# Kernel optimization log

Measured on AMD Instinct MI355X. Metric: run time of the kernel, lower is better.

The kernel has to match this reference:

```python
import jax, jax.numpy as jnp
import numpy as np

N_USER, N_ITEM, D = 50000, 30000, 64
N = N_USER + N_ITEM
NNZ_UI, NNZ_R, NNZ_II = 1000000, 800000, 300000
IMG_F, TXT_F = 512, 384
EPS = 1e-5


def spmm(rows, cols, vals, x, n_out):
    # sparse [n_out, n_in] @ dense [n_in, d] via gather + segment-sum
    return jax.ops.segment_sum(vals[:, None] * x[cols], rows, num_segments=n_out)


def leaky_relu(x):
    return jnp.where(x >= 0, x, 0.01 * x)


def setup_inputs() -> dict:
    key = jax.random.key(0)
    ks = jax.random.split(key, 32)
    f = lambda i, shape, s=0.05: (jax.random.normal(ks[i], shape, dtype=jnp.float32) * s)
    inp = {
        'user_emb': f(0, (N_USER, D)),
        'item_emb': f(1, (N_ITEM, D)),
        'image_embedding': f(2, (N_ITEM, IMG_F), 1.0),
        'text_embedding': f(3, (N_ITEM, TXT_F), 1.0),
        'W_img': f(4, (IMG_F, D)), 'b_img': jnp.zeros((D,), jnp.float32),
        'bn_g_img': jnp.ones((D,), jnp.float32), 'bn_b_img': jnp.zeros((D,), jnp.float32),
        'W_txt': f(5, (TXT_F, D)), 'b_txt': jnp.zeros((D,), jnp.float32),
        'bn_g_txt': jnp.ones((D,), jnp.float32), 'bn_b_txt': jnp.zeros((D,), jnp.float32),
        'W_gate_img': f(6, (D, D)), 'b_gate_img': jnp.zeros((D,), jnp.float32),
        'W_gate_txt': f(7, (D, D)), 'b_gate_txt': jnp.zeros((D,), jnp.float32),
        'W_common1': f(8, (D, D)), 'b_common1': jnp.zeros((D,), jnp.float32),
        'w_common2': f(9, (D,)),
        'ui_vals': jax.random.uniform(ks[10], (NNZ_UI,), dtype=jnp.float32),
        'R_vals': jax.random.uniform(ks[11], (NNZ_R,), dtype=jnp.float32),
        'ii_img_vals': jax.random.uniform(ks[12], (NNZ_II,), dtype=jnp.float32),
        'ii_txt_vals': jax.random.uniform(ks[13], (NNZ_II,), dtype=jnp.float32),
        'ui_rows': jax.random.randint(ks[14], (NNZ_UI,), 0, N, dtype=jnp.int32),
        'ui_cols': jax.random.randint(ks[15], (NNZ_UI,), 0, N, dtype=jnp.int32),
        'R_rows': jax.random.randint(ks[16], (NNZ_R,), 0, N_USER, dtype=jnp.int32),
        'R_cols': jax.random.randint(ks[17], (NNZ_R,), 0, N_ITEM, dtype=jnp.int32),
        'ii_img_rows': jax.random.randint(ks[18], (NNZ_II,), 0, N_ITEM, dtype=jnp.int32),
        'ii_img_cols': jax.random.randint(ks[19], (NNZ_II,), 0, N_ITEM, dtype=jnp.int32),
        'ii_txt_rows': jax.random.randint(ks[20], (NNZ_II,), 0, N_ITEM, dtype=jnp.int32),
        'ii_txt_cols': jax.random.randint(ks[21], (NNZ_II,), 0, N_ITEM, dtype=jnp.int32),
    }
    return inp


def reference(user_emb, item_emb, image_embedding, text_embedding,
              W_img, b_img, bn_g_img, bn_b_img,
              W_txt, b_txt, bn_g_txt, bn_b_txt,
              W_gate_img, b_gate_img, W_gate_txt, b_gate_txt,
              W_common1, b_common1, w_common2,
              ui_vals, R_vals, ii_img_vals, ii_txt_vals,
              ui_rows, ui_cols, R_rows, R_cols,
              ii_img_rows, ii_img_cols, ii_txt_rows, ii_txt_cols):
    # ---- user_item_GCN: adj = original + diffusion (fused edge list) ----
    cat = jnp.concatenate([item_emb, user_emb], axis=0)  # [N, D], item first per source
    embs = [cat]
    for _ in range(2):
        cat = spmm(ui_rows, ui_cols, ui_vals, cat, N)
        embs.append(cat)
    content_embedding = jnp.stack(embs, axis=1).mean(axis=1)  # [N, D]

    # ---- modal projections (BN inference, dropout=eval identity) ----
    def project(x, W, b, g, beta):
        h = x @ W + b
        h = h * (g / jnp.sqrt(1.0 + EPS)) + beta  # BatchNorm1d, running stats (0, 1)
        return leaky_relu(h)

    img_feat = project(image_embedding, W_img, b_img, bn_g_img, bn_b_img)  # [I, D]
    txt_feat = project(text_embedding, W_txt, b_txt, bn_g_txt, bn_b_txt)

    # ---- item_item_GCN ----
    def modal_branch(feat, Wg, bg, rows, cols, vals):
        it = item_emb * jax.nn.sigmoid(feat @ Wg + bg)  # gated item embedding
        for _ in range(2):
            it = spmm(rows, cols, vals, it, N_ITEM)
        us = spmm(R_rows, R_cols, R_vals, it, N_USER)  # R @ item -> user
        return jnp.concatenate([us, it], axis=0)  # [N, D], user first per source

    image_ui = modal_branch(img_feat, W_gate_img, b_gate_img, ii_img_rows, ii_img_cols, ii_img_vals)
    text_ui = modal_branch(txt_feat, W_gate_txt, b_gate_txt, ii_txt_rows, ii_txt_cols, ii_txt_vals)

    # ---- gate_attention_fusion (non-tiktok: 2 modalities) ----
    def att_score(e):
        return leaky_relu(e @ W_common1 + b_common1) @ w_common2  # [N]

    att = jnp.stack([att_score(image_ui), att_score(text_ui)], axis=-1)  # [N, 2]
    w = jax.nn.softmax(att, axis=-1)
    common = w[:, 0:1] * image_ui + w[:, 1:2] * text_ui
    special_img = image_ui - common
    special_txt = text_ui - common

    return jnp.stack([content_embedding, special_img, special_txt, common], axis=0)  # [4, N, D]
```

## Files before the change

### kernel.cpp

```cpp
#include <hip/hip_runtime.h>

#define N_USER 50000
#define N_ITEM 30000
#define DIM    64
#define NTOT   80000
#define NNZ_UI 1000000
#define NNZ_R  800000
#define NNZ_II 300000
#define IMG_F  512
#define TXT_F  384

#define NROWS_ALL 190000
#define NNZ_ALL   2400000
#define BASE_R    NTOT
#define BASE_II   (NTOT + N_USER)
#define BASE_IT   (NTOT + N_USER + N_ITEM)

#define RB_BITS   9
#define RB_ROWS   512
#define NBUCK     ((NROWS_ALL + RB_ROWS - 1) / RB_ROWS)
#define NBLK_A2   400
#define EDG_A2    6000

__device__ __forceinline__ int edge_row(int i,
        const int* __restrict__ r0, const int* __restrict__ r1,
        const int* __restrict__ r2, const int* __restrict__ r3){
    if (i < NNZ_UI)                       return r0[i];
    if (i < NNZ_UI + NNZ_R)               return BASE_R  + r1[i - NNZ_UI];
    if (i < NNZ_UI + NNZ_R + NNZ_II)      return BASE_II + r2[i - NNZ_UI - NNZ_R];
    return BASE_IT + r3[i - NNZ_UI - NNZ_R - NNZ_II];
}

__device__ __forceinline__ void edge_all(int i,
        const int* __restrict__ r0, const int* __restrict__ c0, const float* __restrict__ v0,
        const int* __restrict__ r1, const int* __restrict__ c1, const float* __restrict__ v1,
        const int* __restrict__ r2, const int* __restrict__ c2, const float* __restrict__ v2,
        const int* __restrict__ r3, const int* __restrict__ c3, const float* __restrict__ v3,
        int& gr, int& col, float& val){
    if (i < NNZ_UI){
        gr = r0[i]; col = c0[i]; val = v0[i];
    } else if (i < NNZ_UI + NNZ_R){
        int j = i - NNZ_UI;               gr = BASE_R  + r1[j]; col = c1[j]; val = v1[j];
    } else if (i < NNZ_UI + NNZ_R + NNZ_II){
        int j = i - NNZ_UI - NNZ_R;       gr = BASE_II + r2[j]; col = c2[j]; val = v2[j];
    } else {
        int j = i - NNZ_UI - NNZ_R - NNZ_II; gr = BASE_IT + r3[j]; col = c3[j]; val = v3[j];
    }
}

__global__ __launch_bounds__(256) void k_bhist(const int* __restrict__ r0,
        const int* __restrict__ r1, const int* __restrict__ r2,
        const int* __restrict__ r3, int* __restrict__ bcnt){
    __shared__ int h[NBUCK];
    for (int i = threadIdx.x; i < NBUCK; i += 256) h[i] = 0;
    __syncthreads();
    const int stride = gridDim.x * 256;
    for (int i = blockIdx.x * 256 + threadIdx.x; i < NNZ_ALL; i += stride){
        int gr = edge_row(i, r0, r1, r2, r3);
        atomicAdd(&h[gr >> RB_BITS], 1);
    }
    __syncthreads();
    for (int i = threadIdx.x; i < NBUCK; i += 256){
        int c = h[i];
        if (c) atomicAdd(&bcnt[i], c);
    }
}

__global__ __launch_bounds__(512) void k_bscan(const int* __restrict__ bcnt,
        int* __restrict__ bbase, int* __restrict__ off){
    __shared__ int sh[512];
    const int t = threadIdx.x;
    int v = (t < NBUCK) ? bcnt[t] : 0;
    sh[t] = v;
    __syncthreads();
    for (int d = 1; d < 512; d <<= 1){
        int u = (t >= d) ? sh[t - d] : 0;
        __syncthreads();
        sh[t] += u;
        __syncthreads();
    }
    if (t < NBUCK) bbase[t] = sh[t] - v;
    if (t == NBUCK - 1){
        bbase[NBUCK] = sh[t];
        off[NROWS_ALL] = sh[t];
    }
}

__global__ __launch_bounds__(256) void k_bin(
        const int* __restrict__ r0, const int* __restrict__ c0, const float* __restrict__ v0,
        const int* __restrict__ r1, const int* __restrict__ c1, const float* __restrict__ v1,
        const int* __restrict__ r2, const int* __restrict__ c2, const float* __restrict__ v2,
        const int* __restrict__ r3, const int* __restrict__ c3, const float* __restrict__ v3,
        const int* __restrict__ bbase, int* __restrict__ bcur,
        int2* __restrict__ binned){
    __shared__ int lofs[NBUCK];
    __shared__ int lcur[NBUCK];
    const int t = threadIdx.x;
    for (int i = t; i < NBUCK; i += 256){ lofs[i] = 0; lcur[i] = 0; }
    __syncthreads();
    const int s0 = blockIdx.x * EDG_A2, s1 = s0 + EDG_A2;
    for (int i = s0 + t; i < s1; i += 256){
        int gr = edge_row(i, r0, r1, r2, r3);
        atomicAdd(&lofs[gr >> RB_BITS], 1);
    }
    __syncthreads();
    for (int i = t; i < NBUCK; i += 256){
        int c = lofs[i];
        lofs[i] = c ? (bbase[i] + atomicAdd(&bcur[i], c)) : 0;
    }
    __syncthreads();
    for (int i = s0 + t; i < s1; i += 256){
        int gr, col; float val;
        edge_all(i, r0, c0, v0, r1, c1, v1, r2, c2, v2, r3, c3, v3, gr, col, val);
        int b = gr >> RB_BITS;
        int slot = atomicAdd(&lcur[b], 1);
        binned[lofs[b] + slot] = make_int2((col << RB_BITS) | (gr & (RB_ROWS - 1)),
                                           __float_as_int(val));
    }
}

__global__ __launch_bounds__(256) void k_scatter(const int* __restrict__ bbase,
        const int2* __restrict__ binned, int* __restrict__ off,
        int2* __restrict__ csr){
    __shared__ int h[RB_ROWS];
    const int t = threadIdx.x;
    const int b = blockIdx.x;
    const int base = bbase[b];
    const int nb = bbase[b + 1] - base;
    h[t] = 0; h[t + 256] = 0;
    __syncthreads();
    for (int i = t; i < nb; i += 256)
        atomicAdd(&h[binned[base + i].x & (RB_ROWS - 1)], 1);
    __syncthreads();
    if (t < 64){
        int v[8], s = 0;
#pragma unroll
        for (int k = 0; k < 8; ++k){ v[k] = h[t * 8 + k]; s += v[k]; }
        int incl = s;
#pragma unroll
        for (int d = 1; d < 64; d <<= 1){
            int u = __shfl_up(incl, d, 64);
            if (t >= d) incl += u;
        }
        int run = incl - s;
#pragma unroll
        for (int k = 0; k < 8; ++k){ int tmp = v[k]; h[t * 8 + k] = run; run += tmp; }
    }
    __syncthreads();
    const int row0 = b << RB_BITS;
    for (int i = t; i < RB_ROWS; i += 256){
        int r = row0 + i;
        if (r < NROWS_ALL) off[r] = base + h[i];
    }
    __syncthreads();
    for (int i = t; i < nb; i += 256){
        int2 rec = binned[base + i];
        int lr = rec.x & (RB_ROWS - 1);
        int slot = atomicAdd(&h[lr], 1);
        csr[base + slot] = make_int2(rec.x >> RB_BITS, rec.y);
    }
}

__global__ void k_cat0(const float* __restrict__ item, const float* __restrict__ user,
                       float* __restrict__ o1){
    int i = blockIdx.x * 256 + threadIdx.x;
    const int ITEMS = N_ITEM * DIM;
    o1[i] = (i < ITEMS) ? item[i] : user[i - ITEMS];
}

__global__ void k_pull(const int* __restrict__ off, const int2* __restrict__ csr,
                       const float* __restrict__ x, float* __restrict__ y, int nrows){
    int t = blockIdx.x * 256 + threadIdx.x;
    int r = t >> 4;
    if (r >= nrows) return;
    int l = (t & 15) << 2;
    int s = off[r], e = off[r + 1];
    float4 a0 = {0.f, 0.f, 0.f, 0.f};
    float4 a1 = {0.f, 0.f, 0.f, 0.f};
    int j = s;
    for (; j + 2 <= e; j += 2){
        int2 e0 = csr[j];
        int2 e1 = csr[j + 1];
        float v0 = __int_as_float(e0.y);
        float v1 = __int_as_float(e1.y);
        const float4 x0 = *reinterpret_cast<const float4*>(x + ((long)e0.x << 6) + l);
        const float4 x1 = *reinterpret_cast<const float4*>(x + ((long)e1.x << 6) + l);
        a0.x = fmaf(v0, x0.x, a0.x);
        a0.y = fmaf(v0, x0.y, a0.y);
        a0.z = fmaf(v0, x0.z, a0.z);
        a0.w = fmaf(v0, x0.w, a0.w);
        a1.x = fmaf(v1, x1.x, a1.x);
        a1.y = fmaf(v1, x1.y, a1.y);
        a1.z = fmaf(v1, x1.z, a1.z);
        a1.w = fmaf(v1, x1.w, a1.w);
    }
    if (j < e){
        int2 e0 = csr[j];
        float v0 = __int_as_float(e0.y);
        const float4 x0 = *reinterpret_cast<const float4*>(x + ((long)e0.x << 6) + l);
        a0.x = fmaf(v0, x0.x, a0.x);
        a0.y = fmaf(v0, x0.y, a0.y);
        a0.z = fmaf(v0, x0.z, a0.z);
        a0.w = fmaf(v0, x0.w, a0.w);
    }
    a0.x += a1.x; a0.y += a1.y; a0.z += a1.z; a0.w += a1.w;
    *reinterpret_cast<float4*>(y + ((long)r << 6) + l) = a0;
}

__global__ void k_content(const float* __restrict__ a, const float* __restrict__ b,
                          const float* __restrict__ c, float* __restrict__ o0){
    int i = blockIdx.x * 256 + threadIdx.x;
    o0[i] = (a[i] + b[i] + c[i]) * (1.0f / 3.0f);
}

template<int K>
__global__ __launch_bounds__(256) void k_projgate(
        const float* __restrict__ X,
        const float* __restrict__ W,  const float* __restrict__ b,
        const float* __restrict__ g,  const float* __restrict__ beta,
        const float* __restrict__ Wg, const float* __restrict__ bg,
        const float* __restrict__ item, float* __restrict__ outP){
    __shared__ float xs[48][68];
    __shared__ float ws[64][64];
    const int t  = threadIdx.x;
    const int tr = t >> 4;
    const int tc = t & 15;
    const int row0 = blockIdx.x * 48;

    float acc[3][4];
#pragma unroll
    for (int i = 0; i < 3; ++i)
#pragma unroll
        for (int j = 0; j < 4; ++j) acc[i][j] = 0.f;

    for (int ks = 0; ks < K; ks += 64){
        __syncthreads();
#pragma unroll
        for (int i = 0; i < 3; ++i){
            int r = tr + 16 * i;
            *reinterpret_cast<float4*>(&xs[r][tc * 4]) =
                *reinterpret_cast<const float4*>(X + (long)(row0 + r) * K + ks + tc * 4);
        }
        {
            const float4* wsrc = reinterpret_cast<const float4*>(W + (long)ks * 64);
            float4* wdst = reinterpret_cast<float4*>(&ws[0][0]);
#pragma unroll
            for (int i = 0; i < 4; ++i) wdst[t + 256 * i] = wsrc[t + 256 * i];
        }
        __syncthreads();
#pragma unroll 8
        for (int kk = 0; kk < 64; kk += 2){
            float2 a[3];
#pragma unroll
            for (int i = 0; i < 3; ++i)
                a[i] = *reinterpret_cast<const float2*>(&xs[tr + 16 * i][kk]);
            float4 b0 = *reinterpret_cast<const float4*>(&ws[kk][tc * 4]);
            float4 b1 = *reinterpret_cast<const float4*>(&ws[kk + 1][tc * 4]);
#pragma unroll
            for (int i = 0; i < 3; ++i){
                acc[i][0] = fmaf(a[i].x, b0.x, acc[i][0]);
                acc[i][1] = fmaf(a[i].x, b0.y, acc[i][1]);
                acc[i][2] = fmaf(a[i].x, b0.z, acc[i][2]);
                acc[i][3] = fmaf(a[i].x, b0.w, acc[i][3]);
                acc[i][0] = fmaf(a[i].y, b1.x, acc[i][0]);
                acc[i][1] = fmaf(a[i].y, b1.y, acc[i][1]);
                acc[i][2] = fmaf(a[i].y, b1.z, acc[i][2]);
                acc[i][3] = fmaf(a[i].y, b1.w, acc[i][3]);
            }
        }
    }

    const float4 b4  = reinterpret_cast<const float4*>(b)[tc];
    const float4 g4  = reinterpret_cast<const float4*>(g)[tc];
    const float4 be4 = reinterpret_cast<const float4*>(beta)[tc];
    __syncthreads();
#pragma unroll
    for (int i = 0; i < 3; ++i){
        int r = tr + 16 * i;
        float4 h;
        h.x = (acc[i][0] + b4.x) * (g4.x * 0.99999500003749943f) + be4.x;
        h.y = (acc[i][1] + b4.y) * (g4.y * 0.99999500003749943f) + be4.y;
        h.z = (acc[i][2] + b4.z) * (g4.z * 0.99999500003749943f) + be4.z;
        h.w = (acc[i][3] + b4.w) * (g4.w * 0.99999500003749943f) + be4.w;
        h.x = (h.x >= 0.f) ? h.x : 0.01f * h.x;
        h.y = (h.y >= 0.f) ? h.y : 0.01f * h.y;
        h.z = (h.z >= 0.f) ? h.z : 0.01f * h.z;
        h.w = (h.w >= 0.f) ? h.w : 0.01f * h.w;
        *reinterpret_cast<float4*>(&xs[r][tc * 4]) = h;
    }
    {
        const float4* wsrc = reinterpret_cast<const float4*>(Wg);
        float4* wdst = reinterpret_cast<float4*>(&ws[0][0]);
#pragma unroll
        for (int i = 0; i < 4; ++i) wdst[t + 256 * i] = wsrc[t + 256 * i];
    }
    __syncthreads();

    float ac2[3][4];
#pragma unroll
    for (int i = 0; i < 3; ++i)
#pragma unroll
        for (int j = 0; j < 4; ++j) ac2[i][j] = 0.f;
#pragma unroll 8
    for (int kk = 0; kk < 64; kk += 2){
        float2 a[3];
#pragma unroll
        for (int i = 0; i < 3; ++i)
            a[i] = *reinterpret_cast<const float2*>(&xs[tr + 16 * i][kk]);
        float4 b0 = *reinterpret_cast<const float4*>(&ws[kk][tc * 4]);
        float4 b1 = *reinterpret_cast<const float4*>(&ws[kk + 1][tc * 4]);
#pragma unroll
        for (int i = 0; i < 3; ++i){
            ac2[i][0] = fmaf(a[i].x, b0.x, ac2[i][0]);
            ac2[i][1] = fmaf(a[i].x, b0.y, ac2[i][1]);
            ac2[i][2] = fmaf(a[i].x, b0.z, ac2[i][2]);
            ac2[i][3] = fmaf(a[i].x, b0.w, ac2[i][3]);
            ac2[i][0] = fmaf(a[i].y, b1.x, ac2[i][0]);
            ac2[i][1] = fmaf(a[i].y, b1.y, ac2[i][1]);
            ac2[i][2] = fmaf(a[i].y, b1.z, ac2[i][2]);
            ac2[i][3] = fmaf(a[i].y, b1.w, ac2[i][3]);
        }
    }

    const float4 bg4 = reinterpret_cast<const float4*>(bg)[tc];
#pragma unroll
    for (int i = 0; i < 3; ++i){
        int r = tr + 16 * i;
        const float4 iv = *reinterpret_cast<const float4*>(
                item + (long)(row0 + r) * 64 + tc * 4);
        float4 o;
        o.x = iv.x / (1.f + __expf(-(ac2[i][0] + bg4.x)));
        o.y = iv.y / (1.f + __expf(-(ac2[i][1] + bg4.y)));
        o.z = iv.z / (1.f + __expf(-(ac2[i][2] + bg4.z)));
        o.w = iv.w / (1.f + __expf(-(ac2[i][3] + bg4.w)));
        *reinterpret_cast<float4*>(outP + (long)(row0 + r) * 64 + tc * 4) = o;
    }
}

__global__ void k_copy(const float* __restrict__ s, float* __restrict__ d){
    int i = blockIdx.x * 256 + threadIdx.x;
    d[i] = s[i];
}

__global__ __launch_bounds__(256) void k_fuse(const float* __restrict__ img,
        const float* __restrict__ txt, const float* __restrict__ W1,
        const float* __restrict__ b1, const float* __restrict__ w2,
        float* __restrict__ out){
    __shared__ float si[4][64], st[4][64];
    const int t = threadIdx.x;
    const int w = t >> 6, c = t & 63;
    const long row = (long)blockIdx.x * 4 + w;
    float ie = img[row * 64 + c];
    float te = txt[row * 64 + c];
    si[w][c] = ie;  st[w][c] = te;
    __syncthreads();
    float ai = 0.f, at = 0.f;
#pragma unroll
    for (int k = 0; k < 64; ++k){
        float wv = W1[k * 64 + c];
        ai = fmaf(si[w][k], wv, ai);
        at = fmaf(st[w][k], wv, at);
    }
    float bb = b1[c];
    float hi = ai + bb; hi = (hi >= 0.f) ? hi : 0.01f * hi;
    float ht = at + bb; ht = (ht >= 0.f) ? ht : 0.01f * ht;
    float wc = w2[c];
    float pi = hi * wc, pt = ht * wc;
#pragma unroll
    for (int m = 1; m < 64; m <<= 1){
        pi += __shfl_xor(pi, m, 64);
        pt += __shfl_xor(pt, m, 64);
    }
    float mx = fmaxf(pi, pt);
    float ei = __expf(pi - mx), et = __expf(pt - mx);
    float inv = 1.f / (ei + et);
    float wi = ei * inv, wt = et * inv;
    float common = wi * ie + wt * te;
    const long NTD = (long)NTOT * DIM;
    long o = row * 64 + c;
    out[NTD + o]     = ie - common;
    out[2 * NTD + o] = te - common;
    out[3 * NTD + o] = common;
}

extern "C" void kernel_launch(void* const* d_in, const int* in_sizes, int n_in,
                              void* d_out, int out_size, void* d_ws, size_t ws_size,
                              hipStream_t stream){
    const float* user_emb  = (const float*)d_in[0];
    const float* item_emb  = (const float*)d_in[1];
    const float* image_emb = (const float*)d_in[2];
    const float* text_emb  = (const float*)d_in[3];
    const float* W_img = (const float*)d_in[4];
    const float* b_img = (const float*)d_in[5];
    const float* g_img = (const float*)d_in[6];
    const float* be_img= (const float*)d_in[7];
    const float* W_txt = (const float*)d_in[8];
    const float* b_txt = (const float*)d_in[9];
    const float* g_txt = (const float*)d_in[10];
    const float* be_txt= (const float*)d_in[11];
    const float* W_gi  = (const float*)d_in[12];
    const float* b_gi  = (const float*)d_in[13];
    const float* W_gt  = (const float*)d_in[14];
    const float* b_gt  = (const float*)d_in[15];
    const float* W_c1  = (const float*)d_in[16];
    const float* b_c1  = (const float*)d_in[17];
    const float* w_c2  = (const float*)d_in[18];
    const float* ui_vals = (const float*)d_in[19];
    const float* R_vals  = (const float*)d_in[20];
    const float* ii_iv   = (const float*)d_in[21];
    const float* ii_tv   = (const float*)d_in[22];
    const int* ui_rows = (const int*)d_in[23];
    const int* ui_cols = (const int*)d_in[24];
    const int* R_rows  = (const int*)d_in[25];
    const int* R_cols  = (const int*)d_in[26];
    const int* ii_ir   = (const int*)d_in[27];
    const int* ii_ic   = (const int*)d_in[28];
    const int* ii_tr   = (const int*)d_in[29];
    const int* ii_tc   = (const int*)d_in[30];

    const long ND = (long)NTOT * DIM;
    const long ID = (long)N_ITEM * DIM;
    const long UD = (long)N_USER * DIM;

    float* out = (float*)d_out;
    float* o0 = out;
    float* o1 = out + ND;
    float* o2 = out + 2 * ND;
    float* o3 = out + 3 * ND;

    float* P = o3;
    float* Q = o3 + ID;

    int2* binned = (int2*)o0;

    int2* csr   = (int2*)d_ws;
    int*  off   = (int*)(csr + NNZ_ALL);
    int*  bcnt  = off + NROWS_ALL + 4;
    int*  bcur  = bcnt + NBUCK;
    int*  bbase = bcur + NBUCK;

    hipMemsetAsync(bcnt, 0, 2 * NBUCK * sizeof(int), stream);
    k_bhist<<<512, 256, 0, stream>>>(ui_rows, R_rows, ii_ir, ii_tr, bcnt);
    k_bscan<<<1, 512, 0, stream>>>(bcnt, bbase, off);
    k_bin<<<NBLK_A2, 256, 0, stream>>>(
        ui_rows, ui_cols, ui_vals,  R_rows, R_cols, R_vals,
        ii_ir, ii_ic, ii_iv,        ii_tr, ii_tc, ii_tv,
        bbase, bcur, binned);
    k_scatter<<<NBUCK, 256, 0, stream>>>(bbase, binned, off, csr);

    const int* offUI = off;
    const int* offR  = off + BASE_R;
    const int* offI2 = off + BASE_II;
    const int* offT2 = off + BASE_IT;

    k_cat0<<<ND / 256, 256, 0, stream>>>(item_emb, user_emb, o1);
    k_pull<<<NTOT / 16, 256, 0, stream>>>(offUI, csr, o1, o2, NTOT);
    k_pull<<<NTOT / 16, 256, 0, stream>>>(offUI, csr, o2, o3, NTOT);
    k_content<<<ND / 256, 256, 0, stream>>>(o1, o2, o3, o0);

    k_projgate<IMG_F><<<N_ITEM / 48, 256, 0, stream>>>(
        image_emb, W_img, b_img, g_img, be_img, W_gi, b_gi, item_emb, P);
    k_pull<<<N_ITEM / 16, 256, 0, stream>>>(offI2, csr, P, Q, N_ITEM);
    k_pull<<<N_ITEM / 16, 256, 0, stream>>>(offI2, csr, Q, P, N_ITEM);
    k_pull<<<N_USER / 16, 256, 0, stream>>>(offR, csr, P, o1, N_USER);
    k_copy<<<ID / 256, 256, 0, stream>>>(P, o1 + UD);

    k_projgate<TXT_F><<<N_ITEM / 48, 256, 0, stream>>>(
        text_emb, W_txt, b_txt, g_txt, be_txt, W_gt, b_gt, item_emb, P);
    k_pull<<<N_ITEM / 16, 256, 0, stream>>>(offT2, csr, P, Q, N_ITEM);
    k_pull<<<N_ITEM / 16, 256, 0, stream>>>(offT2, csr, Q, P, N_ITEM);
    k_pull<<<N_USER / 16, 256, 0, stream>>>(offR, csr, P, o2, N_USER);
    k_copy<<<ID / 256, 256, 0, stream>>>(P, o2 + UD);

    k_fuse<<<NTOT / 4, 256, 0, stream>>>(o1, o2, W_c1, b_c1, w_c2, out);
}
```

Measured before the change: 636.7 us.

## Fuse content mean into second pull, drop copies, register-tile attention fusion

The second UI propagation pass now computes the three-layer mean in the same kernel, which removes the separate content kernel and the write and reread of o3. The second item-item pull now writes straight into the concat buffers, so the two copy kernels go away. The attention fusion kernel is rewritten to handle 64 rows per block, with W1 staged in shared memory and a 4x4 register-tiled matmul that uses float4 loads and stores. This cuts global W1 rereads and the one-row-per-wave inefficiency, at the cost of more shared memory and more registers per block.

```diff
diff --git a/kernel.cpp b/kernel.cpp
--- a/kernel.cpp
+++ b/kernel.cpp
@@ -207,10 +207,50 @@
     *reinterpret_cast<float4*>(y + ((long)r << 6) + l) = a0;
 }
 
-__global__ void k_content(const float* __restrict__ a, const float* __restrict__ b,
-                          const float* __restrict__ c, float* __restrict__ o0){
-    int i = blockIdx.x * 256 + threadIdx.x;
-    o0[i] = (a[i] + b[i] + c[i]) * (1.0f / 3.0f);
+__global__ void k_pull_mean(const int* __restrict__ off, const int2* __restrict__ csr,
+                            const float* __restrict__ x, const float* __restrict__ a,
+                            float* __restrict__ o0, int nrows){
+    int t = blockIdx.x * 256 + threadIdx.x;
+    int r = t >> 4;
+    if (r >= nrows) return;
+    int l = (t & 15) << 2;
+    int s = off[r], e = off[r + 1];
+    float4 a0 = {0.f, 0.f, 0.f, 0.f};
+    float4 a1 = {0.f, 0.f, 0.f, 0.f};
+    int j = s;
+    for (; j + 2 <= e; j += 2){
+        int2 e0 = csr[j];
+        int2 e1 = csr[j + 1];
+        float v0 = __int_as_float(e0.y);
+        float v1 = __int_as_float(e1.y);
+        const float4 x0 = *reinterpret_cast<const float4*>(x + ((long)e0.x << 6) + l);
+        const float4 x1 = *reinterpret_cast<const float4*>(x + ((long)e1.x << 6) + l);
+        a0.x = fmaf(v0, x0.x, a0.x);
+        a0.y = fmaf(v0, x0.y, a0.y);
+        a0.z = fmaf(v0, x0.z, a0.z);
+        a0.w = fmaf(v0, x0.w, a0.w);
+        a1.x = fmaf(v1, x1.x, a1.x);
+        a1.y = fmaf(v1, x1.y, a1.y);
+        a1.z = fmaf(v1, x1.z, a1.z);
+        a1.w = fmaf(v1, x1.w, a1.w);
+    }
+    if (j < e){
+        int2 e0 = csr[j];
+        float v0 = __int_as_float(e0.y);
+        const float4 x0 = *reinterpret_cast<const float4*>(x + ((long)e0.x << 6) + l);
+        a0.x = fmaf(v0, x0.x, a0.x);
+        a0.y = fmaf(v0, x0.y, a0.y);
+        a0.z = fmaf(v0, x0.z, a0.z);
+        a0.w = fmaf(v0, x0.w, a0.w);
+    }
+    const float4 av = *reinterpret_cast<const float4*>(a + ((long)r << 6) + l);
+    const float4 xv = *reinterpret_cast<const float4*>(x + ((long)r << 6) + l);
+    float4 o;
+    o.x = (av.x + xv.x + a0.x + a1.x) * (1.0f / 3.0f);
+    o.y = (av.y + xv.y + a0.y + a1.y) * (1.0f / 3.0f);
+    o.z = (av.z + xv.z + a0.z + a1.z) * (1.0f / 3.0f);
+    o.w = (av.w + xv.w + a0.w + a1.w) * (1.0f / 3.0f);
+    *reinterpret_cast<float4*>(o0 + ((long)r << 6) + l) = o;
 }
 
 template<int K>
@@ -337,50 +377,114 @@
     }
 }
 
-__global__ void k_copy(const float* __restrict__ s, float* __restrict__ d){
-    int i = blockIdx.x * 256 + threadIdx.x;
-    d[i] = s[i];
-}
-
 __global__ __launch_bounds__(256) void k_fuse(const float* __restrict__ img,
         const float* __restrict__ txt, const float* __restrict__ W1,
         const float* __restrict__ b1, const float* __restrict__ w2,
         float* __restrict__ out){
-    __shared__ float si[4][64], st[4][64];
-    const int t = threadIdx.x;
-    const int w = t >> 6, c = t & 63;
-    const long row = (long)blockIdx.x * 4 + w;
-    float ie = img[row * 64 + c];
-    float te = txt[row * 64 + c];
-    si[w][c] = ie;  st[w][c] = te;
-    __syncthreads();
-    float ai = 0.f, at = 0.f;
-#pragma unroll
-    for (int k = 0; k < 64; ++k){
-        float wv = W1[k * 64 + c];
-        ai = fmaf(si[w][k], wv, ai);
-        at = fmaf(st[w][k], wv, at);
-    }
-    float bb = b1[c];
-    float hi = ai + bb; hi = (hi >= 0.f) ? hi : 0.01f * hi;
-    float ht = at + bb; ht = (ht >= 0.f) ? ht : 0.01f * ht;
-    float wc = w2[c];
-    float pi = hi * wc, pt = ht * wc;
-#pragma unroll
-    for (int m = 1; m < 64; m <<= 1){
-        pi += __shfl_xor(pi, m, 64);
-        pt += __shfl_xor(pt, m, 64);
-    }
-    float mx = fmaxf(pi, pt);
-    float ei = __expf(pi - mx), et = __expf(pt - mx);
-    float inv = 1.f / (ei + et);
-    float wi = ei * inv, wt = et * inv;
-    float common = wi * ie + wt * te;
+    __shared__ float si[64][68];
+    __shared__ float st[64][68];
+    __shared__ float w1s[64][64];
+    const int t  = threadIdx.x;
+    const int tr = t >> 4;
+    const int tc = t & 15;
+    const long row0 = (long)blockIdx.x * 64;
+
+#pragma unroll
+    for (int i = 0; i < 4; ++i){
+        int r = tr + 16 * i;
+        *reinterpret_cast<float4*>(&si[r][tc * 4]) =
+            *reinterpret_cast<const float4*>(img + (row0 + r) * 64 + tc * 4);
+        *reinterpret_cast<float4*>(&st[r][tc * 4]) =
+            *reinterpret_cast<const float4*>(txt + (row0 + r) * 64 + tc * 4);
+    }
+    {
+        const float4* wsrc = reinterpret_cast<const float4*>(W1);
+        float4* wdst = reinterpret_cast<float4*>(&w1s[0][0]);
+#pragma unroll
+        for (int i = 0; i < 4; ++i) wdst[t + 256 * i] = wsrc[t + 256 * i];
+    }
+    __syncthreads();
+
+    float ai[4][4], at[4][4];
+#pragma unroll
+    for (int i = 0; i < 4; ++i)
+#pragma unroll
+        for (int j = 0; j < 4; ++j){ ai[i][j] = 0.f; at[i][j] = 0.f; }
+
+#pragma unroll 8
+    for (int kk = 0; kk < 64; kk += 2){
+        float4 b0 = *reinterpret_cast<const float4*>(&w1s[kk][tc * 4]);
+        float4 b1v = *reinterpret_cast<const float4*>(&w1s[kk + 1][tc * 4]);
+#pragma unroll
+        for (int i = 0; i < 4; ++i){
+            float2 a = *reinterpret_cast<const float2*>(&si[tr + 16 * i][kk]);
+            float2 c = *reinterpret_cast<const float2*>(&st[tr + 16 * i][kk]);
+            ai[i][0] = fmaf(a.x, b0.x, ai[i][0]);
+            ai[i][1] = fmaf(a.x, b0.y, ai[i][1]);
+            ai[i][2] = fmaf(a.x, b0.z, ai[i][2]);
+            ai[i][3] = fmaf(a.x, b0.w, ai[i][3]);
+            ai[i][0] = fmaf(a.y, b1v.x, ai[i][0]);
+            ai[i][1] = fmaf(a.y, b1v.y, ai[i][1]);
+            ai[i][2] = fmaf(a.y, b1v.z, ai[i][2]);
+            ai[i][3] = fmaf(a.y, b1v.w, ai[i][3]);
+            at[i][0] = fmaf(c.x, b0.x, at[i][0]);
+            at[i][1] = fmaf(c.x, b0.y, at[i][1]);
+            at[i][2] = fmaf(c.x, b0.z, at[i][2]);
+            at[i][3] = fmaf(c.x, b0.w, at[i][3]);
+            at[i][0] = fmaf(c.y, b1v.x, at[i][0]);
+            at[i][1] = fmaf(c.y, b1v.y, at[i][1]);
+            at[i][2] = fmaf(c.y, b1v.z, at[i][2]);
+            at[i][3] = fmaf(c.y, b1v.w, at[i][3]);
+        }
+    }
+
+    const float4 b14 = reinterpret_cast<const float4*>(b1)[tc];
+    const float4 w24 = reinterpret_cast<const float4*>(w2)[tc];
+    float pi[4], pt[4];
+#pragma unroll
+    for (int i = 0; i < 4; ++i){
+        float hi0 = ai[i][0] + b14.x; hi0 = (hi0 >= 0.f) ? hi0 : 0.01f * hi0;
+        float hi1 = ai[i][1] + b14.y; hi1 = (hi1 >= 0.f) ? hi1 : 0.01f * hi1;
+        float hi2 = ai[i][2] + b14.z; hi2 = (hi2 >= 0.f) ? hi2 : 0.01f * hi2;
+        float hi3 = ai[i][3] + b14.w; hi3 = (hi3 >= 0.f) ? hi3 : 0.01f * hi3;
+        float ht0 = at[i][0] + b14.x; ht0 = (ht0 >= 0.f) ? ht0 : 0.01f * ht0;
+        float ht1 = at[i][1] + b14.y; ht1 = (ht1 >= 0.f) ? ht1 : 0.01f * ht1;
+        float ht2 = at[i][2] + b14.z; ht2 = (ht2 >= 0.f) ? ht2 : 0.01f * ht2;
+        float ht3 = at[i][3] + b14.w; ht3 = (ht3 >= 0.f) ? ht3 : 0.01f * ht3;
+        pi[i] = fmaf(hi0, w24.x, fmaf(hi1, w24.y, fmaf(hi2, w24.z, hi3 * w24.w)));
+        pt[i] = fmaf(ht0, w24.x, fmaf(ht1, w24.y, fmaf(ht2, w24.z, ht3 * w24.w)));
+    }
+#pragma unroll
+    for (int m = 1; m < 16; m <<= 1){
+#pragma unroll
+        for (int i = 0; i < 4; ++i){
+            pi[i] += __shfl_xor(pi[i], m, 64);
+            pt[i] += __shfl_xor(pt[i], m, 64);
+        }
+    }
+
     const long NTD = (long)NTOT * DIM;
-    long o = row * 64 + c;
-    out[NTD + o]     = ie - common;
-    out[2 * NTD + o] = te - common;
-    out[3 * NTD + o] = common;
+#pragma unroll
+    for (int i = 0; i < 4; ++i){
+        int r = tr + 16 * i;
+        float mx = fmaxf(pi[i], pt[i]);
+        float ei = __expf(pi[i] - mx), et = __expf(pt[i] - mx);
+        float inv = 1.f / (ei + et);
+        float wi = ei * inv, wt = et * inv;
+        const float4 ie = *reinterpret_cast<const float4*>(&si[r][tc * 4]);
+        const float4 te = *reinterpret_cast<const float4*>(&st[r][tc * 4]);
+        float4 cm, oi, ot;
+        cm.x = wi * ie.x + wt * te.x;
+        cm.y = wi * ie.y + wt * te.y;
+        cm.z = wi * ie.z + wt * te.z;
+        cm.w = wi * ie.w + wt * te.w;
+        oi.x = ie.x - cm.x; oi.y = ie.y - cm.y; oi.z = ie.z - cm.z; oi.w = ie.w - cm.w;
+        ot.x = te.x - cm.x; ot.y = te.y - cm.y; ot.z = te.z - cm.z; ot.w = te.w - cm.w;
+        long o = (row0 + r) * 64 + tc * 4;
+        *reinterpret_cast<float4*>(out + NTD + o)     = oi;
+        *reinterpret_cast<float4*>(out + 2 * NTD + o) = ot;
+        *reinterpret_cast<float4*>(out + 3 * NTD + o) = cm;
+    }
 }
 
 extern "C" void kernel_launch(void* const* d_in, const int* in_sizes, int n_in,
@@ -455,22 +559,19 @@
 
     k_cat0<<<ND / 256, 256, 0, stream>>>(item_emb, user_emb, o1);
     k_pull<<<NTOT / 16, 256, 0, stream>>>(offUI, csr, o1, o2, NTOT);
-    k_pull<<<NTOT / 16, 256, 0, stream>>>(offUI, csr, o2, o3, NTOT);
-    k_content<<<ND / 256, 256, 0, stream>>>(o1, o2, o3, o0);
+    k_pull_mean<<<NTOT / 16, 256, 0, stream>>>(offUI, csr, o2, o1, o0, NTOT);
 
     k_projgate<IMG_F><<<N_ITEM / 48, 256, 0, stream>>>(
         image_emb, W_img, b_img, g_img, be_img, W_gi, b_gi, item_emb, P);
     k_pull<<<N_ITEM / 16, 256, 0, stream>>>(offI2, csr, P, Q, N_ITEM);
-    k_pull<<<N_ITEM / 16, 256, 0, stream>>>(offI2, csr, Q, P, N_ITEM);
-    k_pull<<<N_USER / 16, 256, 0, stream>>>(offR, csr, P, o1, N_USER);
-    k_copy<<<ID / 256, 256, 0, stream>>>(P, o1 + UD);
+    k_pull<<<N_ITEM / 16, 256, 0, stream>>>(offI2, csr, Q, o1 + UD, N_ITEM);
+    k_pull<<<N_USER / 16, 256, 0, stream>>>(offR, csr, o1 + UD, o1, N_USER);
 
     k_projgate<TXT_F><<<N_ITEM / 48, 256, 0, stream>>>(
         text_emb, W_txt, b_txt, g_txt, be_txt, W_gt, b_gt, item_emb, P);
     k_pull<<<N_ITEM / 16, 256, 0, stream>>>(offT2, csr, P, Q, N_ITEM);
-    k_pull<<<N_ITEM / 16, 256, 0, stream>>>(offT2, csr, Q, P, N_ITEM);
-    k_pull<<<N_USER / 16, 256, 0, stream>>>(offR, csr, P, o2, N_USER);
-    k_copy<<<ID / 256, 256, 0, stream>>>(P, o2 + UD);
-
-    k_fuse<<<NTOT / 4, 256, 0, stream>>>(o1, o2, W_c1, b_c1, w_c2, out);
-}
+    k_pull<<<N_ITEM / 16, 256, 0, stream>>>(offT2, csr, Q, o2 + UD, N_ITEM);
+    k_pull<<<N_USER / 16, 256, 0, stream>>>(offR, csr, o2 + UD, o2, N_USER);
+
+    k_fuse<<<NTOT / 64, 256, 0, stream>>>(o1, o2, W_c1, b_c1, w_c2, out);
+}
```

After: 592.5 us. -6.9%, faster.
